# Kernel tuning notes

Measured on AMD Instinct MI355X. Metric: run time of the kernel, lower is better.

The kernel has to match this reference:

```python
import jax, jax.numpy as jnp
import numpy as np

S = 2048
HIDDEN = 4096
NH, NKV, HD = 32, 8, 128
QPK = NH // NKV  # 4
BLOCK, LOCAL, VERT = 64, 16, 8
ROPE_BASE = 1.0e6
SCALE = 1.0 / HD  # mup scaling: head_dim / mup_attn_multiplier(=1.0)


def setup_inputs() -> dict:
    key = jax.random.key(0)
    ks = jax.random.split(key, 5)
    qkv_out = NKV * (QPK + 2) * HD  # 6144, head-major layout
    return {
        "positions": jnp.arange(S, dtype=jnp.int32),
        "hidden_states": jax.random.normal(ks[0], (S, HIDDEN), jnp.float32),
        "w_qkv": jax.random.normal(ks[1], (qkv_out, HIDDEN), jnp.float32) * 0.02,
        "b_qkv": jax.random.normal(ks[2], (qkv_out,), jnp.float32) * 0.02,
        "w_dense": jax.random.normal(ks[3], (HIDDEN, HIDDEN), jnp.float32) * 0.02,
        "b_dense": jax.random.normal(ks[4], (HIDDEN,), jnp.float32) * 0.02,
    }


def _rope(x, cos, sin):
    # NeoX-style (non-interleaved) rotary over full head_dim.
    # x: [S, n_heads, HD]; cos/sin: [S, HD//2]
    d2 = x.shape[-1] // 2
    x1, x2 = x[..., :d2], x[..., d2:]
    c, s = cos[:, None, :], sin[:, None, :]
    return jnp.concatenate([x1 * c - x2 * s, x2 * c + x1 * s], axis=-1)


def _blocksparse_mask(positions):
    # vllm phi3small pattern: block (qb,kb) active iff causal AND
    # (qb-kb < local_blocks OR (kb + head + 1) % vert_stride == 0), hetero heads.
    qb = positions // BLOCK                       # [S]
    heads = jnp.arange(NH, dtype=positions.dtype)
    diff = qb[:, None] - qb[None, :]              # [S,S]
    local = diff < LOCAL                          # [S,S]
    vert = ((qb[None, None, :] + heads[:, None, None] + 1) % VERT) == 0  # [NH,1,S]
    causal = positions[:, None] >= positions[None, :]                     # [S,S]
    return (local[None] | vert) & causal[None]    # [NH,S,S]


def reference(positions, hidden_states, w_qkv, b_qkv, w_dense, b_dense):
    seq = hidden_states.shape[0]
    qkv = hidden_states @ w_qkv.T + b_qkv                   # [S, 6144]
    qkv = qkv.reshape(seq, NKV, QPK + 2, HD)                # head-major split
    q = qkv[:, :, :QPK].reshape(seq, NH, HD)
    k = qkv[:, :, QPK]                                      # [S, NKV, HD]
    v = qkv[:, :, QPK + 1]

    pos = positions.astype(jnp.float32)  # rope_position_scale = 1.0
    inv_freq = 1.0 / (ROPE_BASE ** (jnp.arange(0, HD, 2, dtype=jnp.float32) / HD))
    freqs = pos[:, None] * inv_freq                          # [S, HD/2]
    cos, sin = jnp.cos(freqs), jnp.sin(freqs)
    q = _rope(q, cos, sin)
    k = _rope(k, cos, sin)

    # GQA: each kv head serves QPK query heads
    kx = jnp.repeat(k, QPK, axis=1)                          # [S, NH, HD]
    vx = jnp.repeat(v, QPK, axis=1)

    scores = jnp.einsum('qhd,khd->hqk', q, kx) * SCALE       # [NH,S,S]
    mask = _blocksparse_mask(positions)
    scores = jnp.where(mask, scores, -jnp.inf)  # diag always in local block -> no empty rows
    p = jax.nn.softmax(scores, axis=-1)
    out = jnp.einsum('hqk,khd->qhd', p, vx).reshape(seq, NH * HD)
    return out @ w_dense.T + b_dense
```

## Files before the change

kernel.cpp:

```cpp
#include <hip/hip_runtime.h>

#define S_LEN   2048
#define HID     4096
#define NHEADS  32
#define NKVH    8
#define HDIM    128
#define NQKV    6144
#define ATT_SCALE (1.0f/128.0f)

typedef unsigned short u16;
typedef __attribute__((ext_vector_type(8))) __bf16 bf16x8;
typedef __attribute__((ext_vector_type(4))) float  f32x4;

__device__ __forceinline__ u16 f2bf(float f) {
    union { float f; unsigned u; } x; x.f = f;
    unsigned u = x.u;
    u += 0x7fffu + ((u >> 16) & 1u);
    return (u16)(u >> 16);
}
__device__ __forceinline__ float bf2f(u16 v) {
    union { unsigned u; float f; } x; x.u = ((unsigned)v) << 16; return x.f;
}

__global__ __launch_bounds__(256) void cvt_bf16_kernel(const float* __restrict__ in,
                                                       u16* __restrict__ out, int n4) {
    int stride = gridDim.x * blockDim.x;
    for (int i = blockIdx.x * blockDim.x + threadIdx.x; i < n4; i += stride) {
        float4 v = *(const float4*)(in + (size_t)i * 4);
        ushort4 o = make_ushort4(f2bf(v.x), f2bf(v.y), f2bf(v.z), f2bf(v.w));
        *(ushort4*)(out + (size_t)i * 4) = o;
    }
}

#define BM 128
#define BN 128
#define BK 32

template <bool OUT_BF16>
__global__ __launch_bounds__(256) void gemm_bt_kernel(
    const u16* __restrict__ A,
    const u16* __restrict__ B,
    const float* __restrict__ bias,
    void* __restrict__ Cout,
    int M, int N, int K)
{
    __shared__ u16 Alds[2][BM][BK];
    __shared__ u16 Blds[2][BN][BK];

    const int tid  = threadIdx.x;
    const int wid  = tid >> 6;
    const int lane = tid & 63;
    const int ln   = lane & 15;
    const int quad = lane >> 4;
    const int wm   = (wid >> 1) * 64;
    const int wn   = (wid & 1) * 64;
    const int tileM = blockIdx.y * BM;
    const int tileN = blockIdx.x * BN;

    const int srow = lane >> 2;
    const int scol = ((lane & 3) ^ ((srow >> 1) & 3)) * 8;

    f32x4 acc[4][4];
    #pragma unroll
    for (int i = 0; i < 4; i++)
        #pragma unroll
        for (int j = 0; j < 4; j++) {
            f32x4 z = {0.f, 0.f, 0.f, 0.f};
            acc[i][j] = z;
        }

    auto stage = [&](int k, int buf) {
        const int k0 = k * BK;
        #pragma unroll
        for (int p = 0; p < 2; p++) {
            int r = p * 64 + wid * 16;
            const u16* ga = A + (size_t)(tileM + r + srow) * K + k0 + scol;
            const u16* gb = B + (size_t)(tileN + r + srow) * K + k0 + scol;
            __builtin_amdgcn_global_load_lds(
                (const __attribute__((address_space(1))) void*)ga,
                (__attribute__((address_space(3))) void*)&Alds[buf][r][0], 16, 0, 0);
            __builtin_amdgcn_global_load_lds(
                (const __attribute__((address_space(1))) void*)gb,
                (__attribute__((address_space(3))) void*)&Blds[buf][r][0], 16, 0, 0);
        }
    };

    const int nIter = K / BK;
    stage(0, 0);

    const int pc = (quad ^ ((ln >> 1) & 3)) * 8;

    for (int k = 0; k < nIter; k++) {
        const int buf = k & 1;
        __syncthreads();
        if (k + 1 < nIter) stage(k + 1, buf ^ 1);

        bf16x8 af[4], bfr[4];
        #pragma unroll
        for (int i = 0; i < 4; i++)
            af[i] = *(const bf16x8*)(&Alds[buf][wm + i * 16 + ln][pc]);
        #pragma unroll
        for (int j = 0; j < 4; j++)
            bfr[j] = *(const bf16x8*)(&Blds[buf][wn + j * 16 + ln][pc]);
        #pragma unroll
        for (int i = 0; i < 4; i++)
            #pragma unroll
            for (int j = 0; j < 4; j++)
                acc[i][j] = __builtin_amdgcn_mfma_f32_16x16x32_bf16(af[i], bfr[j], acc[i][j], 0, 0, 0);
    }

    #pragma unroll
    for (int i = 0; i < 4; i++) {
        #pragma unroll
        for (int j = 0; j < 4; j++) {
            int n = tileN + wn + j * 16 + ln;
            float bv = bias[n];
            #pragma unroll
            for (int r = 0; r < 4; r++) {
                int m = tileM + wm + i * 16 + quad * 4 + r;
                float v = acc[i][j][r] + bv;
                if (OUT_BF16)
                    ((u16*)Cout)[(size_t)m * N + n] = f2bf(v);
                else
                    ((float*)Cout)[(size_t)m * N + n] = v;
            }
        }
    }
}

__global__ __launch_bounds__(128) void rope_split_kernel(
    const u16* __restrict__ qkv, const int* __restrict__ positions,
    u16* __restrict__ qb_o, u16* __restrict__ kb_o, u16* __restrict__ vb_o)
{
    const int d   = threadIdx.x;
    const int pos = blockIdx.x;
    const int hy  = blockIdx.y;
    const float p = (float)positions[pos];

    if (hy >= NHEADS + NKVH) {
        int kv = hy - NHEADS - NKVH;
        const u16* src = qkv + (size_t)pos * NQKV + (kv * 6 + 5) * HDIM;
        vb_o[((size_t)kv * S_LEN + pos) * HDIM + d] = src[d];
        return;
    }
    const u16* src;
    u16* dst;
    if (hy < NHEADS) {
        int kv = hy >> 2, qi = hy & 3;
        src = qkv + (size_t)pos * NQKV + (kv * 6 + qi) * HDIM;
        dst = qb_o + ((size_t)hy * S_LEN + pos) * HDIM;
    } else {
        int kv = hy - NHEADS;
        src = qkv + (size_t)pos * NQKV + (kv * 6 + 4) * HDIM;
        dst = kb_o + ((size_t)kv * S_LEN + pos) * HDIM;
    }
    int d2 = d & 63;
    float inv = expf(-(float)d2 * (13.815510557964274f / 64.0f));
    float fr = p * inv;
    float s, c;
    sincosf(fr, &s, &c);
    float x1 = bf2f(src[d2]);
    float x2 = bf2f(src[d2 + 64]);
    float o = (d < 64) ? (x1 * c - x2 * s) : (x2 * c + x1 * s);
    dst[d] = f2bf(o);
}

#define LDK 136
#define LDV 72
__global__ __launch_bounds__(256) void attn_bs_kernel(
    const u16* __restrict__ Q,
    const u16* __restrict__ K,
    const u16* __restrict__ V,
    u16* __restrict__ O)
{
    __shared__ u16 Qs[64][LDK];
    __shared__ u16 Ks[64][LDK];
    __shared__ u16 Vt[128][LDV];
    __shared__ u16 Ps[4][16][LDV];

    const int qb = blockIdx.x;
    const int h  = blockIdx.y;
    const int kv = h >> 2;
    const int tid  = threadIdx.x;
    const int w    = tid >> 6;
    const int lane = tid & 63;
    const int ln   = lane & 15;
    const int quad = lane >> 4;

    const u16* Qg = Q + ((size_t)h * S_LEN + qb * 64) * HDIM;
    {
        int col = (tid & 15) * 8;
        #pragma unroll
        for (int p = 0; p < 4; p++) {
            int row = p * 16 + (tid >> 4);
            *(uint4*)(&Qs[row][col]) = *(const uint4*)(Qg + row * HDIM + col);
        }
    }

    f32x4 oacc[8];
    #pragma unroll
    for (int n = 0; n < 8; n++) { f32x4 z = {0.f,0.f,0.f,0.f}; oacc[n] = z; }
    float mrow[4] = {-1e30f, -1e30f, -1e30f, -1e30f};
    float lrow[4] = {0.f, 0.f, 0.f, 0.f};

    for (int kb = 0; kb <= qb; kb++) {
        bool sel = (qb - kb < 16) || (((kb + h + 1) & 7) == 0);
        if (!sel) continue;

        __syncthreads();
        const u16* Kg = K + ((size_t)kv * S_LEN + kb * 64) * HDIM;
        const u16* Vg = V + ((size_t)kv * S_LEN + kb * 64) * HDIM;
        {
            int col = (tid & 15) * 8;
            #pragma unroll
            for (int p = 0; p < 4; p++) {
                int row = p * 16 + (tid >> 4);
                *(uint4*)(&Ks[row][col]) = *(const uint4*)(Kg + row * HDIM + col);
            }
            int key = tid & 63;
            int dbase = (tid >> 6) * 32;
            #pragma unroll
            for (int p = 0; p < 4; p++) {
                int d0 = dbase + p * 8;
                uint4 vv = *(const uint4*)(Vg + key * HDIM + d0);
                const u16* pv = (const u16*)&vv;
                #pragma unroll
                for (int jj = 0; jj < 8; jj++) Vt[d0 + jj][key] = pv[jj];
            }
        }
        __syncthreads();

        f32x4 sacc[4];
        #pragma unroll
        for (int jj = 0; jj < 4; jj++) { f32x4 z = {0.f,0.f,0.f,0.f}; sacc[jj] = z; }
        #pragma unroll
        for (int ks = 0; ks < 4; ks++) {
            bf16x8 aq = *(const bf16x8*)(&Qs[w * 16 + ln][ks * 32 + quad * 8]);
            #pragma unroll
            for (int jj = 0; jj < 4; jj++) {
                bf16x8 bk = *(const bf16x8*)(&Ks[jj * 16 + ln][ks * 32 + quad * 8]);
                sacc[jj] = __builtin_amdgcn_mfma_f32_16x16x32_bf16(aq, bk, sacc[jj], 0, 0, 0);
            }
        }

        #pragma unroll
        for (int r = 0; r < 4; r++) {
            float pv[4];
            float mx = -1e30f;
            const int qrow = w * 16 + quad * 4 + r;
            #pragma unroll
            for (int jj = 0; jj < 4; jj++) {
                float s = sacc[jj][r] * ATT_SCALE;
                if (kb == qb && (jj * 16 + ln) > qrow) s = -1e30f;
                pv[jj] = s;
                mx = fmaxf(mx, s);
            }
            #pragma unroll
            for (int off = 1; off < 16; off <<= 1)
                mx = fmaxf(mx, __shfl_xor(mx, off, 64));
            float mnew  = fmaxf(mrow[r], mx);
            float alpha = __expf(mrow[r] - mnew);
            float sum = 0.f;
            #pragma unroll
            for (int jj = 0; jj < 4; jj++) {
                float pe = __expf(pv[jj] - mnew);
                pv[jj] = pe;
                sum += pe;
            }
            #pragma unroll
            for (int off = 1; off < 16; off <<= 1)
                sum += __shfl_xor(sum, off, 64);
            lrow[r] = lrow[r] * alpha + sum;
            mrow[r] = mnew;
            #pragma unroll
            for (int n = 0; n < 8; n++) oacc[n][r] *= alpha;
            #pragma unroll
            for (int jj = 0; jj < 4; jj++)
                Ps[w][quad * 4 + r][jj * 16 + ln] = f2bf(pv[jj]);
        }
        __syncthreads();

        #pragma unroll
        for (int kk = 0; kk < 2; kk++) {
            bf16x8 ap = *(const bf16x8*)(&Ps[w][ln][kk * 32 + quad * 8]);
            #pragma unroll
            for (int n = 0; n < 8; n++) {
                bf16x8 bv = *(const bf16x8*)(&Vt[n * 16 + ln][kk * 32 + quad * 8]);
                oacc[n] = __builtin_amdgcn_mfma_f32_16x16x32_bf16(ap, bv, oacc[n], 0, 0, 0);
            }
        }
    }

    #pragma unroll
    for (int n = 0; n < 8; n++) {
        #pragma unroll
        for (int r = 0; r < 4; r++) {
            int row = w * 16 + quad * 4 + r;
            int pos = qb * 64 + row;
            float o = oacc[n][r] / lrow[r];
            O[(size_t)pos * (NHEADS * HDIM) + h * HDIM + n * 16 + ln] = f2bf(o);
        }
    }
}

extern "C" void kernel_launch(void* const* d_in, const int* in_sizes, int n_in,
                              void* d_out, int out_size, void* d_ws, size_t ws_size,
                              hipStream_t stream) {
    const int*   positions = (const int*)d_in[0];
    const float* hidden    = (const float*)d_in[1];
    const float* w_qkv     = (const float*)d_in[2];
    const float* b_qkv     = (const float*)d_in[3];
    const float* w_dense   = (const float*)d_in[4];
    const float* b_dense   = (const float*)d_in[5];
    float* out = (float*)d_out;

    char* ws = (char*)d_ws;
    u16* ws_h    = (u16*)(ws);
    u16* ws_wqkv = (u16*)(ws + 16777216);
    u16* ws_wd   = (u16*)(ws + 67108864);
    u16* ws_qkv  = (u16*)(ws + 100663296);
    u16* ws_q    = (u16*)(ws + 125829120);
    u16* ws_k    = (u16*)(ws + 142606336);
    u16* ws_v    = (u16*)(ws + 146800640);
    u16* ws_attn = (u16*)(ws + 150994944);

    cvt_bf16_kernel<<<1024, 256, 0, stream>>>(hidden,  ws_h,    (S_LEN * HID) / 4);
    cvt_bf16_kernel<<<2048, 256, 0, stream>>>(w_qkv,   ws_wqkv, (NQKV * HID) / 4);
    cvt_bf16_kernel<<<2048, 256, 0, stream>>>(w_dense, ws_wd,   (HID * HID) / 4);

    gemm_bt_kernel<true><<<dim3(NQKV / BN, S_LEN / BM), 256, 0, stream>>>(
        ws_h, ws_wqkv, b_qkv, ws_qkv, S_LEN, NQKV, HID);

    rope_split_kernel<<<dim3(S_LEN, NHEADS + 2 * NKVH), 128, 0, stream>>>(
        ws_qkv, positions, ws_q, ws_k, ws_v);

    attn_bs_kernel<<<dim3(S_LEN / 64, NHEADS), 256, 0, stream>>>(ws_q, ws_k, ws_v, ws_attn);

    gemm_bt_kernel<false><<<dim3(HID / BN, S_LEN / BM), 256, 0, stream>>>(
        ws_attn, ws_wd, b_dense, out, S_LEN, HID, HID);
}
```

Before: 579.8 us.

## Pre-transpose V, keep Q in registers, and prefetch K/V tiles in attention

A new kernel writes V into a transposed [kv][d][pos] layout, so the attention kernel can copy V tiles into shared memory with vector stores. The old path did a scalar transposing scatter into shared memory. The attention loop now loads the next selected K/V block into registers while the current block computes, which overlaps global loads with the MFMA work. Q fragments are held in registers instead of shared memory, and the barrier before the per-wave P·V step is dropped. The cost is an extra kernel launch plus more register pressure from the prefetch buffers.

Result: slower. 647.3 us (+11.6%).

```diff
diff --git a/kernel.cpp b/kernel.cpp
--- a/kernel.cpp
+++ b/kernel.cpp
@@ -130,19 +130,13 @@
 
 __global__ __launch_bounds__(128) void rope_split_kernel(
     const u16* __restrict__ qkv, const int* __restrict__ positions,
-    u16* __restrict__ qb_o, u16* __restrict__ kb_o, u16* __restrict__ vb_o)
+    u16* __restrict__ qb_o, u16* __restrict__ kb_o)
 {
     const int d   = threadIdx.x;
     const int pos = blockIdx.x;
     const int hy  = blockIdx.y;
     const float p = (float)positions[pos];
 
-    if (hy >= NHEADS + NKVH) {
-        int kv = hy - NHEADS - NKVH;
-        const u16* src = qkv + (size_t)pos * NQKV + (kv * 6 + 5) * HDIM;
-        vb_o[((size_t)kv * S_LEN + pos) * HDIM + d] = src[d];
-        return;
-    }
     const u16* src;
     u16* dst;
     if (hy < NHEADS) {
@@ -165,15 +159,50 @@
     dst[d] = f2bf(o);
 }
 
+__global__ __launch_bounds__(256) void v_transpose_kernel(
+    const u16* __restrict__ qkv, u16* __restrict__ vT)
+{
+    __shared__ u16 Ls[64][136];
+    const int tile = blockIdx.x;
+    const int kvh  = blockIdx.y;
+    const int tid  = threadIdx.x;
+
+    {
+        int r = tid >> 4;
+        int c = (tid & 15) * 8;
+        #pragma unroll
+        for (int p = 0; p < 4; p++) {
+            int row = p * 16 + r;
+            *(uint4*)(&Ls[row][c]) =
+                *(const uint4*)(qkv + (size_t)(tile * 64 + row) * NQKV + (kvh * 6 + 5) * HDIM + c);
+        }
+    }
+    __syncthreads();
+    {
+        int l = tid & 7;
+        int pos0 = l * 8;
+        #pragma unroll
+        for (int p = 0; p < 4; p++) {
+            int d = p * 32 + (tid >> 3);
+            u16 tmp[8];
+            #pragma unroll
+            for (int j = 0; j < 8; j++) {
+                int jj = (j + l) & 7;
+                tmp[jj] = Ls[pos0 + jj][d];
+            }
+            *(uint4*)(vT + ((size_t)kvh * HDIM + d) * S_LEN + tile * 64 + pos0) = *(uint4*)tmp;
+        }
+    }
+}
+
 #define LDK 136
 #define LDV 72
 __global__ __launch_bounds__(256) void attn_bs_kernel(
     const u16* __restrict__ Q,
     const u16* __restrict__ K,
-    const u16* __restrict__ V,
+    const u16* __restrict__ VT,
     u16* __restrict__ O)
 {
-    __shared__ u16 Qs[64][LDK];
     __shared__ u16 Ks[64][LDK];
     __shared__ u16 Vt[128][LDV];
     __shared__ u16 Ps[4][16][LDV];
@@ -187,15 +216,39 @@
     const int ln   = lane & 15;
     const int quad = lane >> 4;
 
-    const u16* Qg = Q + ((size_t)h * S_LEN + qb * 64) * HDIM;
+    bf16x8 qf[4];
     {
-        int col = (tid & 15) * 8;
-        #pragma unroll
-        for (int p = 0; p < 4; p++) {
-            int row = p * 16 + (tid >> 4);
-            *(uint4*)(&Qs[row][col]) = *(const uint4*)(Qg + row * HDIM + col);
-        }
-    }
+        const u16* Qg = Q + ((size_t)h * S_LEN + qb * 64 + w * 16 + ln) * HDIM;
+        #pragma unroll
+        for (int ks = 0; ks < 4; ks++)
+            qf[ks] = *(const bf16x8*)(Qg + ks * 32 + quad * 8);
+    }
+
+    const int krow = tid >> 4;
+    const int kcol = (tid & 15) * 8;
+    const int vrow = tid >> 3;
+    const int vcol = (tid & 7) * 8;
+    const u16* Kbase = K  + (size_t)kv * S_LEN * HDIM;
+    const u16* Vbase = VT + (size_t)kv * HDIM * S_LEN;
+
+    uint4 kreg[4], vreg[4];
+    auto prefetch = [&](int kb) {
+        const u16* Kg = Kbase + (size_t)kb * 64 * HDIM;
+        #pragma unroll
+        for (int p = 0; p < 4; p++)
+            kreg[p] = *(const uint4*)(Kg + (size_t)(p * 16 + krow) * HDIM + kcol);
+        #pragma unroll
+        for (int p = 0; p < 4; p++)
+            vreg[p] = *(const uint4*)(Vbase + (size_t)(p * 32 + vrow) * S_LEN + kb * 64 + vcol);
+    };
+    auto commit = [&]() {
+        #pragma unroll
+        for (int p = 0; p < 4; p++)
+            *(uint4*)(&Ks[p * 16 + krow][kcol]) = kreg[p];
+        #pragma unroll
+        for (int p = 0; p < 4; p++)
+            *(uint4*)(&Vt[p * 32 + vrow][vcol]) = vreg[p];
+    };
 
     f32x4 oacc[8];
     #pragma unroll
@@ -203,31 +256,19 @@
     float mrow[4] = {-1e30f, -1e30f, -1e30f, -1e30f};
     float lrow[4] = {0.f, 0.f, 0.f, 0.f};
 
-    for (int kb = 0; kb <= qb; kb++) {
-        bool sel = (qb - kb < 16) || (((kb + h + 1) & 7) == 0);
-        if (!sel) continue;
+    auto sel = [&](int b) { return (qb - b < 16) || (((b + h + 1) & 7) == 0); };
+
+    int kb = 0;
+    while (!sel(kb)) kb++;
+    prefetch(kb);
+
+    while (kb >= 0) {
+        int nkb = -1;
+        for (int b = kb + 1; b <= qb; b++) if (sel(b)) { nkb = b; break; }
 
         __syncthreads();
-        const u16* Kg = K + ((size_t)kv * S_LEN + kb * 64) * HDIM;
-        const u16* Vg = V + ((size_t)kv * S_LEN + kb * 64) * HDIM;
-        {
-            int col = (tid & 15) * 8;
-            #pragma unroll
-            for (int p = 0; p < 4; p++) {
-                int row = p * 16 + (tid >> 4);
-                *(uint4*)(&Ks[row][col]) = *(const uint4*)(Kg + row * HDIM + col);
-            }
-            int key = tid & 63;
-            int dbase = (tid >> 6) * 32;
-            #pragma unroll
-            for (int p = 0; p < 4; p++) {
-                int d0 = dbase + p * 8;
-                uint4 vv = *(const uint4*)(Vg + key * HDIM + d0);
-                const u16* pv = (const u16*)&vv;
-                #pragma unroll
-                for (int jj = 0; jj < 8; jj++) Vt[d0 + jj][key] = pv[jj];
-            }
-        }
+        commit();
+        if (nkb >= 0) prefetch(nkb);
         __syncthreads();
 
         f32x4 sacc[4];
@@ -235,11 +276,10 @@
         for (int jj = 0; jj < 4; jj++) { f32x4 z = {0.f,0.f,0.f,0.f}; sacc[jj] = z; }
         #pragma unroll
         for (int ks = 0; ks < 4; ks++) {
-            bf16x8 aq = *(const bf16x8*)(&Qs[w * 16 + ln][ks * 32 + quad * 8]);
             #pragma unroll
             for (int jj = 0; jj < 4; jj++) {
                 bf16x8 bk = *(const bf16x8*)(&Ks[jj * 16 + ln][ks * 32 + quad * 8]);
-                sacc[jj] = __builtin_amdgcn_mfma_f32_16x16x32_bf16(aq, bk, sacc[jj], 0, 0, 0);
+                sacc[jj] = __builtin_amdgcn_mfma_f32_16x16x32_bf16(qf[ks], bk, sacc[jj], 0, 0, 0);
             }
         }
 
@@ -278,7 +318,6 @@
             for (int jj = 0; jj < 4; jj++)
                 Ps[w][quad * 4 + r][jj * 16 + ln] = f2bf(pv[jj]);
         }
-        __syncthreads();
 
         #pragma unroll
         for (int kk = 0; kk < 2; kk++) {
@@ -289,6 +328,8 @@
                 oacc[n] = __builtin_amdgcn_mfma_f32_16x16x32_bf16(ap, bv, oacc[n], 0, 0, 0);
             }
         }
+
+        kb = nkb;
     }
 
     #pragma unroll
@@ -321,7 +362,7 @@
     u16* ws_qkv  = (u16*)(ws + 100663296);
     u16* ws_q    = (u16*)(ws + 125829120);
     u16* ws_k    = (u16*)(ws + 142606336);
-    u16* ws_v    = (u16*)(ws + 146800640);
+    u16* ws_vT   = (u16*)(ws + 146800640);
     u16* ws_attn = (u16*)(ws + 150994944);
 
     cvt_bf16_kernel<<<1024, 256, 0, stream>>>(hidden,  ws_h,    (S_LEN * HID) / 4);
@@ -331,10 +372,12 @@
     gemm_bt_kernel<true><<<dim3(NQKV / BN, S_LEN / BM), 256, 0, stream>>>(
         ws_h, ws_wqkv, b_qkv, ws_qkv, S_LEN, NQKV, HID);
 
-    rope_split_kernel<<<dim3(S_LEN, NHEADS + 2 * NKVH), 128, 0, stream>>>(
-        ws_qkv, positions, ws_q, ws_k, ws_v);
-
-    attn_bs_kernel<<<dim3(S_LEN / 64, NHEADS), 256, 0, stream>>>(ws_q, ws_k, ws_v, ws_attn);
+    rope_split_kernel<<<dim3(S_LEN, NHEADS + NKVH), 128, 0, stream>>>(
+        ws_qkv, positions, ws_q, ws_k);
+
+    v_transpose_kernel<<<dim3(S_LEN / 64, NKVH), 256, 0, stream>>>(ws_qkv, ws_vT);
+
+    attn_bs_kernel<<<dim3(S_LEN / 64, NHEADS), 256, 0, stream>>>(ws_q, ws_k, ws_vT, ws_attn);
 
     gemm_bt_kernel<false><<<dim3(HID / BN, S_LEN / BM), 256, 0, stream>>>(
         ws_attn, ws_wd, b_dense, out, S_LEN, HID, HID);
```
